# Kernel tuning notes

Measured on AMD Instinct MI355X. Metric: run time of the kernel, lower is better.

## Reference

```python
import jax, jax.numpy as jnp
import numpy as np

N_USERS = 100000
N_ITEMS = 100000
EMB_DIM = 64
N_LAYERS = 3
NNZ = 12800000


def setup_inputs() -> dict:
    key = jax.random.key(0)
    k1, k2, k3, k4, k5 = jax.random.split(key, 5)
    N = N_USERS + N_ITEMS
    rows = jax.random.randint(k1, (NNZ,), 0, N, dtype=jnp.int32)
    cols = jax.random.randint(k2, (NNZ,), 0, N, dtype=jnp.int32)
    vals = jax.random.uniform(k3, (NNZ,), dtype=jnp.float32)
    user_emb = jax.random.normal(k4, (N_USERS, EMB_DIM), dtype=jnp.float32)
    item_emb = jax.random.normal(k5, (N_ITEMS, EMB_DIM), dtype=jnp.float32)
    return {"rows": rows, "cols": cols, "vals": vals,
            "user_emb": user_emb, "item_emb": item_emb}


def _spmm(rows, cols, vals, x, num_segments):
    # sparse (COO) @ dense: gather source rows, scale, scatter-add to dest rows
    gathered = x[cols] * vals[:, None]          # [nnz, d]
    return jax.ops.segment_sum(gathered, rows, num_segments=num_segments)


def reference(rows, cols, vals, user_emb, item_emb):
    N = user_emb.shape[0] + item_emb.shape[0]
    all_emb = jnp.concatenate([user_emb, item_emb], axis=0)  # [N, d]
    # running sum across layer outputs (fused alternative to stack+mean)
    acc = all_emb
    for _ in range(N_LAYERS):
        all_emb = _spmm(rows, cols, vals, all_emb, N)
        acc = acc + all_emb
    final_emb = acc / jnp.asarray(N_LAYERS + 1, dtype=acc.dtype)
    users_emb = final_emb[:user_emb.shape[0]]
    items_emb = final_emb[user_emb.shape[0]:]
    return (users_emb, items_emb)
```

## Files before the change

### kernel.cpp

```cpp
#include <hip/hip_runtime.h>
#include <hip/hip_fp16.h>

#define EMB 64
#define CH 4096
#define CCAP 264192
#define NCHUNK ((CCAP + CH - 1) / CH)
#define FCAP 4736
#define COLBITS 18
#define COLMASK ((1 << COLBITS) - 1)

typedef int iv4 __attribute__((ext_vector_type(4)));



static __global__ __launch_bounds__(256) void passA_kernel(
    const int* __restrict__ rows, const int* __restrict__ cols, const float* __restrict__ vals,
    int* __restrict__ cfill, int2* __restrict__ stA, int2* __restrict__ stB,
    int ncoarseA, int nnz) {
    __shared__ int2 sbuf[CH];
    __shared__ unsigned char sbin[CH];
    __shared__ int histw[4 * 65];
    __shared__ int lpre[64];
    __shared__ int gbase[64];

    const int tid = threadIdx.x;
    const int wv = tid >> 6;
    const int e0 = blockIdx.x * CH;
    const int cnt = min(CH, nnz - e0);

    for (int i = tid; i < 4 * 65; i += 256) histw[i] = 0;
    __syncthreads();

    for (int k = tid; k < cnt; k += 256)
        atomicAdd(&histw[wv * 65 + (rows[e0 + k] >> 12)], 1);
    __syncthreads();

    if (tid < 64) {
        int h0 = histw[tid], h1 = histw[65 + tid], h2 = histw[130 + tid], h3 = histw[195 + tid];
        int tot = h0 + h1 + h2 + h3;
        int x = tot;
#pragma unroll
        for (int d = 1; d < 64; d <<= 1) { int y = __shfl_up(x, d); if (tid >= d) x += y; }
        int ex = x - tot;
        lpre[tid] = ex;
        histw[tid] = ex; histw[65 + tid] = ex + h0;
        histw[130 + tid] = ex + h0 + h1; histw[195 + tid] = ex + h0 + h1 + h2;
        if (tot > 0) gbase[tid] = atomicAdd(&cfill[tid], tot);
    }
    __syncthreads();

    for (int k = tid; k < cnt; k += 256) {
        int i = e0 + k;
        int r = rows[i];
        int b = r >> 12;
        int w = cols[i] | ((r & 4095) << COLBITS);
        int pos = atomicAdd(&histw[wv * 65 + b], 1);
        sbuf[pos] = make_int2(w, __float_as_int(vals[i]));
        sbin[pos] = (unsigned char)b;
    }
    __syncthreads();

    for (int s = tid; s < cnt; s += 256) {
        int b = sbin[s];
        int idx = gbase[b] + (s - lpre[b]);
        if (idx < CCAP) {
            int2* dst = (b < ncoarseA) ? stA + (size_t)b * CCAP
                                       : stB + (size_t)(b - ncoarseA) * CCAP;
            dst[idx] = sbuf[s];
        }
    }
}


static __global__ __launch_bounds__(256) void passB_kernel(
    const int* __restrict__ cfill, int* __restrict__ ffill,
    const int2* __restrict__ stA, const int2* __restrict__ stB,
    int2* __restrict__ fine8, int ncoarseA) {
    __shared__ int2 sbuf[CH];
    __shared__ unsigned char sbin[CH];
    __shared__ int histw[4 * 65];
    __shared__ int lpre[64];
    __shared__ int gbase[64];

    const int tid = threadIdx.x;
    const int wv = tid >> 6;
    const int c = blockIdx.x / NCHUNK;
    const int j = blockIdx.x % NCHUNK;
    int ccount = cfill[c]; if (ccount > CCAP) ccount = CCAP;
    const int e0 = j * CH;
    const int cnt = min(CH, ccount - e0);
    if (cnt <= 0) return;
    const int2* src = (c < ncoarseA) ? stA + (size_t)c * CCAP + e0
                                     : stB + (size_t)(c - ncoarseA) * CCAP + e0;

    for (int i = tid; i < 4 * 65; i += 256) histw[i] = 0;
    __syncthreads();

    for (int k = tid; k < cnt; k += 256)
        atomicAdd(&histw[wv * 65 + ((src[k].x >> 24) & 63)], 1);
    __syncthreads();

    if (tid < 64) {
        int h0 = histw[tid], h1 = histw[65 + tid], h2 = histw[130 + tid], h3 = histw[195 + tid];
        int tot = h0 + h1 + h2 + h3;
        int x = tot;
#pragma unroll
        for (int d = 1; d < 64; d <<= 1) { int y = __shfl_up(x, d); if (tid >= d) x += y; }
        int ex = x - tot;
        lpre[tid] = ex;
        histw[tid] = ex; histw[65 + tid] = ex + h0;
        histw[130 + tid] = ex + h0 + h1; histw[195 + tid] = ex + h0 + h1 + h2;
        if (tot > 0) gbase[tid] = atomicAdd(&ffill[(c << 6) | tid], tot);
    }
    __syncthreads();

    for (int k = tid; k < cnt; k += 256) {
        int2 e = src[k];
        int f = (e.x >> 24) & 63;
        int pos = atomicAdd(&histw[wv * 65 + f], 1);
        sbuf[pos] = e;
        sbin[pos] = (unsigned char)f;
    }
    __syncthreads();

    for (int s = tid; s < cnt; s += 256) {
        int f = sbin[s];
        int idx = gbase[f] + (s - lpre[f]);
        if (idx < FCAP)
            fine8[(size_t)((c << 6) | f) * FCAP + idx] = sbuf[s];
    }
}


static __global__ __launch_bounds__(256) void sort_kernel(
    int2* __restrict__ fine8, const int* __restrict__ ffill,
    int* __restrict__ rp, int* __restrict__ rend, int ntot) {
    __shared__ int2 ebuf[FCAP];
    __shared__ int histw[4 * 65];
    __shared__ int lprs[64];
    __shared__ int lens[64];

    const int f = blockIdx.x;
    const int tid = threadIdx.x;
    const int wv = tid >> 6;
    int cnt = ffill[f]; if (cnt > FCAP - 192) cnt = FCAP - 192;
    int2* reg8 = fine8 + (size_t)f * FCAP;
    int* reg4 = (int*)reg8;

    for (int i = tid; i < 4 * 65; i += 256) histw[i] = 0;
    __syncthreads();

    for (int k = tid; k < cnt; k += 256) {
        int2 e = reg8[k];
        ebuf[k] = e;
        atomicAdd(&histw[wv * 65 + ((e.x >> COLBITS) & 63)], 1);
    }
    __syncthreads();

    if (tid < 64) {
        int h0 = histw[tid], h1 = histw[65 + tid], h2 = histw[130 + tid], h3 = histw[195 + tid];
        int tot = h0 + h1 + h2 + h3;
        int c4 = (tot + 3) & ~3;
        int x = c4;
#pragma unroll
        for (int d = 1; d < 64; d <<= 1) { int y = __shfl_up(x, d); if (tid >= d) x += y; }
        int ex = x - c4;
        lprs[tid] = ex; lens[tid] = tot;
        histw[tid] = ex; histw[65 + tid] = ex + h0;
        histw[130 + tid] = ex + h0 + h1; histw[195 + tid] = ex + h0 + h1 + h2;
    }
    __syncthreads();

    if (tid < 64) {
        int g = f * 64 + tid;
        if (g < ntot) {
            rp[g]   = f * FCAP * 2 + lprs[tid];
            rend[g] = f * FCAP * 2 + lprs[tid] + lens[tid];
        }
    }

    for (int k = tid; k < cnt; k += 256) {
        int2 e = ebuf[k];
        int lr = (e.x >> COLBITS) & 63;
        int pos = atomicAdd(&histw[wv * 65 + lr], 1);
        float v = __int_as_float(e.y);
        int v14 = (int)(v * 16384.f + 0.5f);
        if (v14 > 16383) v14 = 16383;
        reg4[pos] = (int)(((unsigned)(e.x & COLMASK) << 14) | (unsigned)v14);
    }
}


static __global__ void init_kernel(const float4* __restrict__ ue, const float4* __restrict__ ie,
                                   ushort4* __restrict__ xh, float4* __restrict__ acc,
                                   int nu4, int ntot4) {
    int i = blockIdx.x * blockDim.x + threadIdx.x;
    int stride = gridDim.x * blockDim.x;
    for (; i < ntot4; i += stride) {
        float4 v = (i < nu4) ? ue[i] : ie[i - nu4];
        acc[i] = v;
        ushort4 h;
        h.x = __half_as_ushort(__float2half_rn(v.x));
        h.y = __half_as_ushort(__float2half_rn(v.y));
        h.z = __half_as_ushort(__float2half_rn(v.z));
        h.w = __half_as_ushort(__float2half_rn(v.w));
        xh[i] = h;
    }
}


template <int LAST>
static __global__ __launch_bounds__(256, 4) void spmm_kernel(
    const int* __restrict__ stage, const int* __restrict__ rp, const int* __restrict__ rend,
    const __half* __restrict__ x, __half* __restrict__ xn,
    float* __restrict__ acc, int nrows) {
    __shared__ alignas(16) int batch_all[4][256];
    const int tid = threadIdx.x;
    const int lane = tid & 63;
    const int wv = tid >> 6;
    const int wid = blockIdx.x * 4 + wv;
    if (wid >= nrows) return;
    int* batch = batch_all[wv];
    const int beg = rp[wid], end = rend[wid];
    const char* xb = (const char*)x;
    const unsigned laneoff = (lane & 15) << 3;
    const int sub = lane >> 4;
    float s0 = 0.f, s1 = 0.f, s2 = 0.f, s3 = 0.f;

    for (int base = beg; base < end; base += 256) {
        int idx = base + 4 * lane;
        iv4 ee = (iv4){0, 0, 0, 0};
        if (idx + 3 < end) {
            ee = *(const iv4*)(stage + idx);
        } else if (idx < end) {
            ee.x = stage[idx];
            if (idx + 1 < end) ee.y = stage[idx + 1];
            if (idx + 2 < end) ee.z = stage[idx + 2];
        }
        *(iv4*)&batch[4 * lane] = ee;

        int rem = end - base; if (rem > 256) rem = 256;
        int ngr = (rem + 3) >> 2;
        ngr = (ngr + 7) & ~7;
        for (int g0 = 0; g0 < ngr; g0 += 8) {
            int w[8];
#pragma unroll
            for (int u = 0; u < 8; ++u) w[u] = batch[4 * (g0 + u) + sub];
            uint2 h[8]; float v[8];
#pragma unroll
            for (int u = 0; u < 8; ++u) {
                unsigned off = (((unsigned)w[u]) >> 14) << 7;
                h[u] = *(const uint2*)(xb + (off | laneoff));
                v[u] = (float)(w[u] & 16383) * (1.f / 16384.f);
            }
            asm volatile("" ::
                "v"(h[0].x), "v"(h[0].y), "v"(h[1].x), "v"(h[1].y),
                "v"(h[2].x), "v"(h[2].y), "v"(h[3].x), "v"(h[3].y),
                "v"(h[4].x), "v"(h[4].y), "v"(h[5].x), "v"(h[5].y),
                "v"(h[6].x), "v"(h[6].y), "v"(h[7].x), "v"(h[7].y));
#pragma unroll
            for (int u = 0; u < 8; ++u) {
                float2 f01 = __half22float2(*(const __half2*)&h[u].x);
                float2 f23 = __half22float2(*(const __half2*)&h[u].y);
                s0 = fmaf(v[u], f01.x, s0);
                s1 = fmaf(v[u], f01.y, s1);
                s2 = fmaf(v[u], f23.x, s2);
                s3 = fmaf(v[u], f23.y, s3);
            }
        }
    }

    s0 += __shfl_xor(s0, 16); s1 += __shfl_xor(s1, 16);
    s2 += __shfl_xor(s2, 16); s3 += __shfl_xor(s3, 16);
    s0 += __shfl_xor(s0, 32); s1 += __shfl_xor(s1, 32);
    s2 += __shfl_xor(s2, 32); s3 += __shfl_xor(s3, 32);

    if (lane < 16) {
        int o = wid * EMB + 4 * lane;
        float4 a = *(const float4*)(acc + o);
        a.x += s0; a.y += s1; a.z += s2; a.w += s3;
        if (LAST) {
            a.x *= 0.25f; a.y *= 0.25f; a.z *= 0.25f; a.w *= 0.25f;
            *(float4*)(acc + o) = a;
        } else {
            *(float4*)(acc + o) = a;
            __half2 h01 = __floats2half2_rn(s0, s1);
            __half2 h23 = __floats2half2_rn(s2, s3);
            uint2 pk;
            pk.x = *(const unsigned int*)&h01;
            pk.y = *(const unsigned int*)&h23;
            *(uint2*)(xn + o) = pk;
        }
    }
}


extern "C" void kernel_launch(void* const* d_in, const int* in_sizes, int n_in,
                              void* d_out, int out_size, void* d_ws, size_t ws_size,
                              hipStream_t stream) {
    const int* rows = (const int*)d_in[0];
    const int* cols = (const int*)d_in[1];
    const float* vals = (const float*)d_in[2];
    const float* ue = (const float*)d_in[3];
    const float* ie = (const float*)d_in[4];
    float* out = (float*)d_out;

    const int nnz = in_sizes[0];
    const int n_users = in_sizes[3] / EMB;
    const int n_items = in_sizes[4] / EMB;
    const int ntot = n_users + n_items;
    const int ncoarse = (ntot + 4095) >> 12;
    const int nfine = (ntot + 63) >> 6;
    const int nfreg = ncoarse << 6;

    int ncA = (int)(((size_t)out_size * 4) / ((size_t)CCAP * 8));
    if (ncA > ncoarse) ncA = ncoarse;

    char* ws = (char*)d_ws;
    size_t off = 0;
    auto alloc = [&](size_t bytes) -> void* {
        void* p = ws + off;
        off = (off + bytes + 255) & ~(size_t)255;
        return p;
    };
    int2* fine8 = (int2*)alloc((size_t)nfreg * FCAP * 8);
    int2* stB   = (int2*)alloc((size_t)(ncoarse - ncA) * CCAP * 8);
    int* rp    = (int*)alloc((size_t)ntot * 4);
    int* rend  = (int*)alloc((size_t)ntot * 4);
    int* cfill = (int*)alloc(64 * 4);
    int* ffill = (int*)alloc((size_t)nfreg * 4);
    (void)ws_size;

    int2* stA = (int2*)out;
    __half* x0 = (__half*)stB;
    __half* x1 = x0 + (size_t)ntot * EMB;

    (void)hipMemsetAsync(cfill, 0, 64 * 4, stream);
    (void)hipMemsetAsync(ffill, 0, (size_t)nfreg * 4, stream);

    int blkA = (nnz + CH - 1) / CH;
    passA_kernel<<<blkA, 256, 0, stream>>>(rows, cols, vals, cfill, stA, stB, ncA, nnz);
    passB_kernel<<<ncoarse * NCHUNK, 256, 0, stream>>>(cfill, ffill, stA, stB, fine8, ncA);
    sort_kernel<<<nfine, 256, 0, stream>>>(fine8, ffill, rp, rend, ntot);

    init_kernel<<<2048, 256, 0, stream>>>((const float4*)ue, (const float4*)ie,
                                          (ushort4*)x0, (float4*)out,
                                          n_users * EMB / 4, ntot * EMB / 4);

    const int* stage4 = (const int*)fine8;
    int spmm_blocks = (ntot + 3) / 4;
    spmm_kernel<0><<<spmm_blocks, 256, 0, stream>>>(stage4, rp, rend, x0, x1, out, ntot);
    spmm_kernel<0><<<spmm_blocks, 256, 0, stream>>>(stage4, rp, rend, x1, x0, out, ntot);
    spmm_kernel<1><<<spmm_blocks, 256, 0, stream>>>(stage4, rp, rend, x0, nullptr, out, ntot);
}
```

Before: 933.0 us.

## Sub-sort row segments by column slice and use persistent-grid SpMM

The sort kernel now orders each row's nonzeros by an 8-way column-range slice, using a larger histogram, so that gathers within a row touch a narrower region of the embedding table and get better cache locality. The SpMM kernel becomes a grid-stride persistent kernel with 2048 blocks that loop over rows, replacing the one-wave-per-row launch, and it drops the occupancy hint in launch bounds. The extra cost is a larger shared histogram and scan in the sort kernel, plus possible load imbalance from the fixed grid size.

```diff
diff --git a/kernel.cpp b/kernel.cpp
--- a/kernel.cpp
+++ b/kernel.cpp
@@ -8,6 +8,8 @@
 #define FCAP 4736
 #define COLBITS 18
 #define COLMASK ((1 << COLBITS) - 1)
+#define NSL 8
+#define BINS (64 * NSL)
 
 typedef int iv4 __attribute__((ext_vector_type(4)));
 
@@ -136,7 +138,7 @@
     int2* __restrict__ fine8, const int* __restrict__ ffill,
     int* __restrict__ rp, int* __restrict__ rend, int ntot) {
     __shared__ int2 ebuf[FCAP];
-    __shared__ int histw[4 * 65];
+    __shared__ int histw[4 * BINS];
     __shared__ int lprs[64];
     __shared__ int lens[64];
 
@@ -147,27 +149,42 @@
     int2* reg8 = fine8 + (size_t)f * FCAP;
     int* reg4 = (int*)reg8;
 
-    for (int i = tid; i < 4 * 65; i += 256) histw[i] = 0;
+    for (int i = tid; i < 4 * BINS; i += 256) histw[i] = 0;
     __syncthreads();
 
     for (int k = tid; k < cnt; k += 256) {
         int2 e = reg8[k];
         ebuf[k] = e;
-        atomicAdd(&histw[wv * 65 + ((e.x >> COLBITS) & 63)], 1);
+        int lr = (e.x >> COLBITS) & 63;
+        int sl = (e.x & COLMASK) >> 15;
+        atomicAdd(&histw[wv * BINS + lr * NSL + sl], 1);
     }
     __syncthreads();
 
     if (tid < 64) {
-        int h0 = histw[tid], h1 = histw[65 + tid], h2 = histw[130 + tid], h3 = histw[195 + tid];
-        int tot = h0 + h1 + h2 + h3;
+        int h[4][NSL];
+        int tot = 0;
+#pragma unroll
+        for (int s = 0; s < NSL; ++s)
+#pragma unroll
+            for (int w = 0; w < 4; ++w) {
+                h[w][s] = histw[w * BINS + tid * NSL + s];
+                tot += h[w][s];
+            }
         int c4 = (tot + 3) & ~3;
         int x = c4;
 #pragma unroll
         for (int d = 1; d < 64; d <<= 1) { int y = __shfl_up(x, d); if (tid >= d) x += y; }
         int ex = x - c4;
         lprs[tid] = ex; lens[tid] = tot;
-        histw[tid] = ex; histw[65 + tid] = ex + h0;
-        histw[130 + tid] = ex + h0 + h1; histw[195 + tid] = ex + h0 + h1 + h2;
+        int run = ex;
+#pragma unroll
+        for (int s = 0; s < NSL; ++s)
+#pragma unroll
+            for (int w = 0; w < 4; ++w) {
+                histw[w * BINS + tid * NSL + s] = run;
+                run += h[w][s];
+            }
     }
     __syncthreads();
 
@@ -182,7 +199,8 @@
     for (int k = tid; k < cnt; k += 256) {
         int2 e = ebuf[k];
         int lr = (e.x >> COLBITS) & 63;
-        int pos = atomicAdd(&histw[wv * 65 + lr], 1);
+        int sl = (e.x & COLMASK) >> 15;
+        int pos = atomicAdd(&histw[wv * BINS + lr * NSL + sl], 1);
         float v = __int_as_float(e.y);
         int v14 = (int)(v * 16384.f + 0.5f);
         if (v14 > 16383) v14 = 16383;
@@ -210,7 +228,7 @@
 
 
 template <int LAST>
-static __global__ __launch_bounds__(256, 4) void spmm_kernel(
+static __global__ __launch_bounds__(256) void spmm_kernel(
     const int* __restrict__ stage, const int* __restrict__ rp, const int* __restrict__ rend,
     const __half* __restrict__ x, __half* __restrict__ xn,
     float* __restrict__ acc, int nrows) {
@@ -218,78 +236,80 @@
     const int tid = threadIdx.x;
     const int lane = tid & 63;
     const int wv = tid >> 6;
-    const int wid = blockIdx.x * 4 + wv;
-    if (wid >= nrows) return;
     int* batch = batch_all[wv];
-    const int beg = rp[wid], end = rend[wid];
     const char* xb = (const char*)x;
     const unsigned laneoff = (lane & 15) << 3;
     const int sub = lane >> 4;
-    float s0 = 0.f, s1 = 0.f, s2 = 0.f, s3 = 0.f;
-
-    for (int base = beg; base < end; base += 256) {
-        int idx = base + 4 * lane;
-        iv4 ee = (iv4){0, 0, 0, 0};
-        if (idx + 3 < end) {
-            ee = *(const iv4*)(stage + idx);
-        } else if (idx < end) {
-            ee.x = stage[idx];
-            if (idx + 1 < end) ee.y = stage[idx + 1];
-            if (idx + 2 < end) ee.z = stage[idx + 2];
+    const int wstride = gridDim.x * 4;
+
+    for (int wid = blockIdx.x * 4 + wv; wid < nrows; wid += wstride) {
+        const int beg = rp[wid], end = rend[wid];
+        float s0 = 0.f, s1 = 0.f, s2 = 0.f, s3 = 0.f;
+
+        for (int base = beg; base < end; base += 256) {
+            int idx = base + 4 * lane;
+            iv4 ee = (iv4){0, 0, 0, 0};
+            if (idx + 3 < end) {
+                ee = *(const iv4*)(stage + idx);
+            } else if (idx < end) {
+                ee.x = stage[idx];
+                if (idx + 1 < end) ee.y = stage[idx + 1];
+                if (idx + 2 < end) ee.z = stage[idx + 2];
+            }
+            *(iv4*)&batch[4 * lane] = ee;
+
+            int rem = end - base; if (rem > 256) rem = 256;
+            int ngr = (rem + 3) >> 2;
+            ngr = (ngr + 7) & ~7;
+            for (int g0 = 0; g0 < ngr; g0 += 8) {
+                int w[8];
+#pragma unroll
+                for (int u = 0; u < 8; ++u) w[u] = batch[4 * (g0 + u) + sub];
+                uint2 h[8]; float v[8];
+#pragma unroll
+                for (int u = 0; u < 8; ++u) {
+                    unsigned off = (((unsigned)w[u]) >> 14) << 7;
+                    h[u] = *(const uint2*)(xb + (off | laneoff));
+                    v[u] = (float)(w[u] & 16383) * (1.f / 16384.f);
+                }
+                asm volatile("" ::
+                    "v"(h[0].x), "v"(h[0].y), "v"(h[1].x), "v"(h[1].y),
+                    "v"(h[2].x), "v"(h[2].y), "v"(h[3].x), "v"(h[3].y),
+                    "v"(h[4].x), "v"(h[4].y), "v"(h[5].x), "v"(h[5].y),
+                    "v"(h[6].x), "v"(h[6].y), "v"(h[7].x), "v"(h[7].y));
+#pragma unroll
+                for (int u = 0; u < 8; ++u) {
+                    float2 f01 = __half22float2(*(const __half2*)&h[u].x);
+                    float2 f23 = __half22float2(*(const __half2*)&h[u].y);
+                    s0 = fmaf(v[u], f01.x, s0);
+                    s1 = fmaf(v[u], f01.y, s1);
+                    s2 = fmaf(v[u], f23.x, s2);
+                    s3 = fmaf(v[u], f23.y, s3);
+                }
+            }
         }
-        *(iv4*)&batch[4 * lane] = ee;
-
-        int rem = end - base; if (rem > 256) rem = 256;
-        int ngr = (rem + 3) >> 2;
-        ngr = (ngr + 7) & ~7;
-        for (int g0 = 0; g0 < ngr; g0 += 8) {
-            int w[8];
-#pragma unroll
-            for (int u = 0; u < 8; ++u) w[u] = batch[4 * (g0 + u) + sub];
-            uint2 h[8]; float v[8];
-#pragma unroll
-            for (int u = 0; u < 8; ++u) {
-                unsigned off = (((unsigned)w[u]) >> 14) << 7;
-                h[u] = *(const uint2*)(xb + (off | laneoff));
-                v[u] = (float)(w[u] & 16383) * (1.f / 16384.f);
-            }
-            asm volatile("" ::
-                "v"(h[0].x), "v"(h[0].y), "v"(h[1].x), "v"(h[1].y),
-                "v"(h[2].x), "v"(h[2].y), "v"(h[3].x), "v"(h[3].y),
-                "v"(h[4].x), "v"(h[4].y), "v"(h[5].x), "v"(h[5].y),
-                "v"(h[6].x), "v"(h[6].y), "v"(h[7].x), "v"(h[7].y));
-#pragma unroll
-            for (int u = 0; u < 8; ++u) {
-                float2 f01 = __half22float2(*(const __half2*)&h[u].x);
-                float2 f23 = __half22float2(*(const __half2*)&h[u].y);
-                s0 = fmaf(v[u], f01.x, s0);
-                s1 = fmaf(v[u], f01.y, s1);
-                s2 = fmaf(v[u], f23.x, s2);
-                s3 = fmaf(v[u], f23.y, s3);
-            }
-        }
-    }
-
-    s0 += __shfl_xor(s0, 16); s1 += __shfl_xor(s1, 16);
-    s2 += __shfl_xor(s2, 16); s3 += __shfl_xor(s3, 16);
-    s0 += __shfl_xor(s0, 32); s1 += __shfl_xor(s1, 32);
-    s2 += __shfl_xor(s2, 32); s3 += __shfl_xor(s3, 32);
-
-    if (lane < 16) {
-        int o = wid * EMB + 4 * lane;
-        float4 a = *(const float4*)(acc + o);
-        a.x += s0; a.y += s1; a.z += s2; a.w += s3;
-        if (LAST) {
-            a.x *= 0.25f; a.y *= 0.25f; a.z *= 0.25f; a.w *= 0.25f;
-            *(float4*)(acc + o) = a;
-        } else {
-            *(float4*)(acc + o) = a;
-            __half2 h01 = __floats2half2_rn(s0, s1);
-            __half2 h23 = __floats2half2_rn(s2, s3);
-            uint2 pk;
-            pk.x = *(const unsigned int*)&h01;
-            pk.y = *(const unsigned int*)&h23;
-            *(uint2*)(xn + o) = pk;
+
+        s0 += __shfl_xor(s0, 16); s1 += __shfl_xor(s1, 16);
+        s2 += __shfl_xor(s2, 16); s3 += __shfl_xor(s3, 16);
+        s0 += __shfl_xor(s0, 32); s1 += __shfl_xor(s1, 32);
+        s2 += __shfl_xor(s2, 32); s3 += __shfl_xor(s3, 32);
+
+        if (lane < 16) {
+            int o = wid * EMB + 4 * lane;
+            float4 a = *(const float4*)(acc + o);
+            a.x += s0; a.y += s1; a.z += s2; a.w += s3;
+            if (LAST) {
+                a.x *= 0.25f; a.y *= 0.25f; a.z *= 0.25f; a.w *= 0.25f;
+                *(float4*)(acc + o) = a;
+            } else {
+                *(float4*)(acc + o) = a;
+                __half2 h01 = __floats2half2_rn(s0, s1);
+                __half2 h23 = __floats2half2_rn(s2, s3);
+                uint2 pk;
+                pk.x = *(const unsigned int*)&h01;
+                pk.y = *(const unsigned int*)&h23;
+                *(uint2*)(xn + o) = pk;
+            }
         }
     }
 }
@@ -348,8 +368,7 @@
                                           n_users * EMB / 4, ntot * EMB / 4);
 
     const int* stage4 = (const int*)fine8;
-    int spmm_blocks = (ntot + 3) / 4;
-    spmm_kernel<0><<<spmm_blocks, 256, 0, stream>>>(stage4, rp, rend, x0, x1, out, ntot);
-    spmm_kernel<0><<<spmm_blocks, 256, 0, stream>>>(stage4, rp, rend, x1, x0, out, ntot);
-    spmm_kernel<1><<<spmm_blocks, 256, 0, stream>>>(stage4, rp, rend, x0, nullptr, out, ntot);
-}
+    spmm_kernel<0><<<2048, 256, 0, stream>>>(stage4, rp, rend, x0, x1, out, ntot);
+    spmm_kernel<0><<<2048, 256, 0, stream>>>(stage4, rp, rend, x1, x0, out, ntot);
+    spmm_kernel<1><<<2048, 256, 0, stream>>>(stage4, rp, rend, x0, nullptr, out, ntot);
+}
```

After: 1.038 ms. 11.3% more time.
